# Kernel optimization log

Hardware: AMD Instinct MI355X
Metric: run time of the kernel (lower is better)

The kernel has to match this reference:

```python
import jax, jax.numpy as jnp
import numpy as np

WEIGHT = 1.0
SIM_THRESHOLD = 0.8


def setup_inputs() -> dict:
    key = jax.random.key(0)
    k1, k2, k3, k4 = jax.random.split(key, 4)
    B, E, H, C = 8192, 16, 1024, 128  # batch, num_experts, hidden, clusters
    routing_probs = jax.random.normal(k1, (B, E), dtype=jnp.float32)
    # Clustered embeddings so some pairs exceed the similarity threshold:
    # intra-cluster cosine sim ~ 1024/(1024 + 0.09*1024) ~ 0.92 > 0.8.
    centers = jax.random.normal(k2, (C, H), dtype=jnp.float32)
    assign = jax.random.randint(k3, (B,), 0, C)
    input_embeddings = centers[assign] + 0.3 * jax.random.normal(k4, (B, H), dtype=jnp.float32)
    return {"routing_probs": routing_probs, "input_embeddings": input_embeddings}


def reference(routing_probs, input_embeddings):
    B = routing_probs.shape[0]
    # L2-normalize embeddings and build pairwise cosine similarity [B, B]
    emb = input_embeddings / jnp.linalg.norm(input_embeddings, axis=-1, keepdims=True)
    sim = emb @ emb.T
    mask = (sim > SIM_THRESHOLD) & ~jnp.eye(B, dtype=bool)
    # Batch-wide softmax/log_softmax computed once (fuses the per-pair loop)
    L = jax.nn.log_softmax(routing_probs, axis=-1)  # [B, E]
    P = jnp.exp(L)                                   # [B, E]
    neg_entropy = jnp.sum(P * L, axis=-1)            # [B], sum_k p_j log p_j
    # kl[i, j] = KL(P_j || P_i) = sum_k P_j (log P_j - L_i)
    kl = neg_entropy[None, :] - L @ P.T              # [B, B]
    cnt = jnp.sum(mask)
    loss = jnp.where(
        cnt > 0,
        jnp.sum(jnp.where(mask, kl, 0.0)) / jnp.maximum(cnt, 1).astype(kl.dtype),
        jnp.array(0.0, dtype=kl.dtype),
    )
    return WEIGHT * loss
```

## Files before the change

kernel.cpp:

```cpp
#include <hip/hip_runtime.h>
#include <hip/hip_bf16.h>
#include <math.h>

#define B_SZ 8192
#define H_SZ 1024
#define E_SZ 16
#define SIM_THR 0.8f

typedef float floatx4 __attribute__((ext_vector_type(4)));
typedef long  longx2  __attribute__((ext_vector_type(2)));

#define OFF_NE   4096
#define OFF_L    65536
#define OFF_P    (65536 + 524288)
#define OFF_EMB  2097152


__device__ __forceinline__ void gload16(const void* g, void* l) {
    __builtin_amdgcn_global_load_lds(
        (const __attribute__((address_space(1))) void*)g,
        (__attribute__((address_space(3))) void*)l, 16, 0, 0);
}

__global__ void prep_kernel(const float* __restrict__ rp,
                            const float* __restrict__ emb,
                            unsigned char* __restrict__ out8,
                            float* __restrict__ L, float* __restrict__ P,
                            float* __restrict__ ne,
                            float* __restrict__ gsum, unsigned int* __restrict__ gcnt,
                            unsigned int* __restrict__ done) {
    const int b = blockIdx.x;
    if (b < 2048) {
        int r    = b * 4 + (threadIdx.x >> 6);
        int lane = threadIdx.x & 63;
        int kt = lane >> 2, q = lane & 3;
        const float4* row4 = (const float4*)(emb + (size_t)r * H_SZ);
        int f0 = (kt * 64 + q * 8) >> 2;
        float4 a0 = row4[f0],     a1 = row4[f0 + 1];
        float4 b0 = row4[f0 + 8], b1 = row4[f0 + 9];
        float ss = a0.x*a0.x + a0.y*a0.y + a0.z*a0.z + a0.w*a0.w
                 + a1.x*a1.x + a1.y*a1.y + a1.z*a1.z + a1.w*a1.w
                 + b0.x*b0.x + b0.y*b0.y + b0.z*b0.z + b0.w*b0.w
                 + b1.x*b1.x + b1.y*b1.y + b1.z*b1.z + b1.w*b1.w;
#pragma unroll
        for (int off = 32; off > 0; off >>= 1) ss += __shfl_down(ss, off, 64);
        ss = __shfl(ss, 0, 64);
        float inv = rsqrtf(ss);
        unsigned int w0, w1, w2, w3;
        w0 = (unsigned int)__builtin_amdgcn_cvt_pk_fp8_f32(a0.x * inv, a0.y * inv, 0, false);
        w0 = (unsigned int)__builtin_amdgcn_cvt_pk_fp8_f32(a0.z * inv, a0.w * inv, w0, true);
        w1 = (unsigned int)__builtin_amdgcn_cvt_pk_fp8_f32(a1.x * inv, a1.y * inv, 0, false);
        w1 = (unsigned int)__builtin_amdgcn_cvt_pk_fp8_f32(a1.z * inv, a1.w * inv, w1, true);
        w2 = (unsigned int)__builtin_amdgcn_cvt_pk_fp8_f32(b0.x * inv, b0.y * inv, 0, false);
        w2 = (unsigned int)__builtin_amdgcn_cvt_pk_fp8_f32(b0.z * inv, b0.w * inv, w2, true);
        w3 = (unsigned int)__builtin_amdgcn_cvt_pk_fp8_f32(b1.x * inv, b1.y * inv, 0, false);
        w3 = (unsigned int)__builtin_amdgcn_cvt_pk_fp8_f32(b1.z * inv, b1.w * inv, w3, true);
        size_t dst = (size_t)(r >> 4) * 16384 + (size_t)kt * 1024
                   + (size_t)q * 256 + (size_t)(r & 15) * 16;
        uint4 c = {w0, w1, w2, w3};
        *(uint4*)(out8 + dst) = c;
    } else {
        int i = (b - 2048) * 256 + threadIdx.x;
        if (i == 0) { *gsum = 0.f; *gcnt = 0u; *done = 0u; }
        if (i >= B_SZ) return;
        const float* x = rp + i * E_SZ;
        float v[E_SZ];
        float m = -INFINITY;
#pragma unroll
        for (int k = 0; k < E_SZ; k++) { v[k] = x[k]; m = fmaxf(m, v[k]); }
        float s = 0.f;
#pragma unroll
        for (int k = 0; k < E_SZ; k++) s += expf(v[k] - m);
        float lse = m + logf(s);
        float nent = 0.f;
#pragma unroll
        for (int k = 0; k < E_SZ; k++) {
            float l = v[k] - lse;
            float p = expf(l);
            L[i * E_SZ + k] = l;
            P[i * E_SZ + k] = p;
            nent += p * l;
        }
        ne[i] = nent;
    }
}

__device__ __forceinline__ int cnt_range(int lo, int hi, int r, int* first) {
    int lo2 = lo + ((r - lo) & 7);
    *first = lo2;
    return (lo2 > hi) ? 0 : ((hi - lo2) >> 3) + 1;
}

#define GRID_PER_XCD 164
__global__ __launch_bounds__(512, 4)
void sim_kl_kernel(const unsigned char* __restrict__ embL,
                   const float* __restrict__ Lm, const float* __restrict__ Pm,
                   const float* __restrict__ ne,
                   float* __restrict__ gsum, unsigned int* __restrict__ gcnt,
                   unsigned int* __restrict__ done, float* __restrict__ out) {
    __shared__ __align__(16) char As[2][16384];
    __shared__ __align__(16) char Bs[2][8192];
    __shared__ float redf[8];
    __shared__ unsigned int redc[8];

    const int x = blockIdx.x & 7;
    int s = blockIdx.x >> 3;
    int BI = 0, bj = 0;
    bool have = false;
    for (BI = 0; BI < 32; BI++) {
        int lo = 2 * BI, f1, f2;
        int n1 = (lo <= 31) ? cnt_range(lo, 31, x, &f1) : 0;
        int n2 = cnt_range(lo < 32 ? 32 : lo, 63, 7 - x, &f2);
        if (s < n1) { bj = f1 + 8 * s; have = true; break; }
        s -= n1;
        if (s < n2) { bj = f2 + 8 * s; have = true; break; }
        s -= n2;
    }

    const int tid  = threadIdx.x;
    const int lane = tid & 63;
    const int wave = tid >> 6;

    float fsum = 0.f;
    unsigned int lcnt = 0;

    if (have) {
        const int rowI = BI * 256, rowJ = bj * 128;
        const int wrg = (wave >> 1);
        const int wcg = (wave & 1);
        const int quad = lane >> 4;
        const int l16  = lane & 15;

        floatx4 acc[4][4];
#pragma unroll
        for (int mi = 0; mi < 4; mi++)
#pragma unroll
            for (int ni = 0; ni < 4; ni++) {
                floatx4 z = {0.f, 0.f, 0.f, 0.f};
                acc[mi][ni] = z;
            }

        const char* srcA = (const char*)embL + (size_t)(BI * 16 + 2 * wave) * 16384 + lane * 16;
        const char* srcB = (const char*)embL + (size_t)(bj * 8 + wave) * 16384 + lane * 16;
        const int aW = 2 * wave * 1024;
        const int bW = wave * 1024;

        {
            gload16(srcA,         As[0] + aW);
            gload16(srcA + 16384, As[0] + aW + 1024);
            gload16(srcB,         Bs[0] + bW);
        }

        const int aoff = wrg * 4096 + lane * 16;
        const int boff = wcg * 4096 + lane * 16;

        for (int kt = 0; kt < 16; kt++) {
            const int b = kt & 1;
            __syncthreads();
            if (kt + 1 < 16) {
                const int ko = (kt + 1) * 1024;
                gload16(srcA + ko,         As[b ^ 1] + aW);
                gload16(srcA + ko + 16384, As[b ^ 1] + aW + 1024);
                gload16(srcB + ko,         Bs[b ^ 1] + bW);
            }

            longx2 af[4], bfm[4];
#pragma unroll
            for (int mi = 0; mi < 4; mi++)
                af[mi] = *(const longx2*)(As[b] + aoff + mi * 1024);
#pragma unroll
            for (int ni = 0; ni < 4; ni++)
                bfm[ni] = *(const longx2*)(Bs[b] + boff + ni * 1024);
#pragma unroll
            for (int mi = 0; mi < 4; mi++)
#pragma unroll
                for (int ni = 0; ni < 4; ni++) {
                    acc[mi][ni] = __builtin_amdgcn_mfma_f32_16x16x32_fp8_fp8(
                        af[mi].x, bfm[ni].x, acc[mi][ni], 0, 0, 0);
                    acc[mi][ni] = __builtin_amdgcn_mfma_f32_16x16x32_fp8_fp8(
                        af[mi].y, bfm[ni].y, acc[mi][ni], 0, 0, 0);
                }
        }

        __syncthreads();
        unsigned short* wl = (unsigned short*)As + wave * 2048;
        int base = 0;
#pragma unroll
        for (int mi = 0; mi < 4; mi++) {
#pragma unroll
            for (int ni = 0; ni < 4; ni++) {
#pragma unroll
                for (int r = 0; r < 4; r++) {
                    int il = wrg * 64 + mi * 16 + quad * 4 + r;
                    int jl = wcg * 64 + ni * 16 + l16;
                    bool msk = (acc[mi][ni][r] > SIM_THR) && (rowJ + jl > rowI + il);
                    unsigned long long bal = __ballot(msk);
                    if (msk) {
                        int pos = base + __popcll(bal & ((1ull << lane) - 1ull));
                        if (pos < 2048) wl[pos] = (unsigned short)((il << 7) | jl);
                    }
                    base += __popcll(bal);
                }
            }
        }
        if (base > 2048) base = 2048;

        for (int t = lane; t < base; t += 64) {
            int e = wl[t];
            int i = rowI + (e >> 7), j = rowJ + (e & 127);
            const float4* Li4 = (const float4*)(Lm + i * E_SZ);
            const float4* Pj4 = (const float4*)(Pm + j * E_SZ);
            const float4* Lj4 = (const float4*)(Lm + j * E_SZ);
            const float4* Pi4 = (const float4*)(Pm + i * E_SZ);
            float d = 0.f, d2 = 0.f;
#pragma unroll
            for (int q = 0; q < 4; q++) {
                float4 a = Li4[q], bb = Pj4[q];
                d += a.x * bb.x + a.y * bb.y + a.z * bb.z + a.w * bb.w;
                float4 a2 = Lj4[q], b2 = Pi4[q];
                d2 += a2.x * b2.x + a2.y * b2.y + a2.z * b2.z + a2.w * b2.w;
            }
            fsum += (ne[j] - d) + (ne[i] - d2);
            lcnt += 2;
        }
    }

#pragma unroll
    for (int off = 32; off > 0; off >>= 1) {
        fsum += __shfl_down(fsum, off, 64);
        lcnt += __shfl_down(lcnt, off, 64);
    }
    if (lane == 0) { redf[wave] = fsum; redc[wave] = lcnt; }
    __syncthreads();
    if (tid == 0) {
        float sv = 0.f;
        unsigned int c = 0u;
#pragma unroll
        for (int w = 0; w < 8; w++) { sv += redf[w]; c += redc[w]; }
        if (c > 0u) {
            atomicAdd(gsum, sv);
            atomicAdd(gcnt, c);
        }
        __threadfence();
        unsigned int old = atomicAdd(done, 1u);
        if (old == gridDim.x - 1) {
            float S = atomicAdd(gsum, 0.0f);
            unsigned int C = atomicAdd(gcnt, 0u);
            out[0] = (C > 0u) ? (S / (float)C) : 0.f;
        }
    }
}

extern "C" void kernel_launch(void* const* d_in, const int* in_sizes, int n_in,
                              void* d_out, int out_size, void* d_ws, size_t ws_size,
                              hipStream_t stream) {
    const float* rp  = (const float*)d_in[0];
    const float* emb = (const float*)d_in[1];
    float* out = (float*)d_out;

    char* ws = (char*)d_ws;
    float*         gsum = (float*)(ws + 0);
    unsigned int*  gcnt = (unsigned int*)(ws + 4);
    unsigned int*  done = (unsigned int*)(ws + 8);
    float*         ne   = (float*)(ws + OFF_NE);
    float*         Lm   = (float*)(ws + OFF_L);
    float*         Pm   = (float*)(ws + OFF_P);
    unsigned char* embL = (unsigned char*)(ws + OFF_EMB);

    prep_kernel<<<2048 + 32, 256, 0, stream>>>(rp, emb, embL, Lm, Pm, ne, gsum, gcnt, done);
    sim_kl_kernel<<<8 * GRID_PER_XCD, 512, 0, stream>>>(embL, Lm, Pm, ne, gsum, gcnt, done, out);
}
```

Before: 174.2 us.

## Switch similarity GEMM from fp8 to int8 MFMA with LDS-staged prep

Embeddings are quantized to symmetric int8 (scaled by 127 after L2 normalization) instead of fp8. The similarity tiles are computed with the i32 16x16x64 int8 MFMA, and the threshold is compared as an integer (0.8*127^2). The prep kernel now handles 16 rows per block and stages them in LDS so the tiled layout is written with coalesced stores. Together this halves the MFMA instruction count per k-tile and makes prep writes cheaper, at the cost of int8 quantization error near the threshold.

```diff
diff --git a/kernel.cpp b/kernel.cpp
--- a/kernel.cpp
+++ b/kernel.cpp
@@ -5,10 +5,9 @@
 #define B_SZ 8192
 #define H_SZ 1024
 #define E_SZ 16
-#define SIM_THR 0.8f
-
+#define SIM_THR_I 12903
 typedef float floatx4 __attribute__((ext_vector_type(4)));
-typedef long  longx2  __attribute__((ext_vector_type(2)));
+typedef int   intx4   __attribute__((ext_vector_type(4)));
 
 #define OFF_NE   4096
 #define OFF_L    65536
@@ -22,45 +21,58 @@
         (__attribute__((address_space(3))) void*)l, 16, 0, 0);
 }
 
-__global__ void prep_kernel(const float* __restrict__ rp,
-                            const float* __restrict__ emb,
-                            unsigned char* __restrict__ out8,
-                            float* __restrict__ L, float* __restrict__ P,
-                            float* __restrict__ ne,
-                            float* __restrict__ gsum, unsigned int* __restrict__ gcnt,
-                            unsigned int* __restrict__ done) {
+__device__ __forceinline__ unsigned int pack4_i8(float4 v, float s) {
+    int a = (int)rintf(v.x * s), b = (int)rintf(v.y * s);
+    int c = (int)rintf(v.z * s), d = (int)rintf(v.w * s);
+    return (a & 255) | ((b & 255) << 8) | ((c & 255) << 16) | ((d & 255) << 24);
+}
+
+__global__ __launch_bounds__(256)
+void prep_kernel(const float* __restrict__ rp,
+                 const float* __restrict__ emb,
+                 unsigned char* __restrict__ out8,
+                 float* __restrict__ L, float* __restrict__ P,
+                 float* __restrict__ ne,
+                 float* __restrict__ gsum, unsigned int* __restrict__ gcnt,
+                 unsigned int* __restrict__ done) {
     const int b = blockIdx.x;
-    if (b < 2048) {
-        int r    = b * 4 + (threadIdx.x >> 6);
-        int lane = threadIdx.x & 63;
-        int kt = lane >> 2, q = lane & 3;
-        const float4* row4 = (const float4*)(emb + (size_t)r * H_SZ);
-        int f0 = (kt * 64 + q * 8) >> 2;
-        float4 a0 = row4[f0],     a1 = row4[f0 + 1];
-        float4 b0 = row4[f0 + 8], b1 = row4[f0 + 9];
-        float ss = a0.x*a0.x + a0.y*a0.y + a0.z*a0.z + a0.w*a0.w
-                 + a1.x*a1.x + a1.y*a1.y + a1.z*a1.z + a1.w*a1.w
-                 + b0.x*b0.x + b0.y*b0.y + b0.z*b0.z + b0.w*b0.w
-                 + b1.x*b1.x + b1.y*b1.y + b1.z*b1.z + b1.w*b1.w;
-#pragma unroll
-        for (int off = 32; off > 0; off >>= 1) ss += __shfl_down(ss, off, 64);
-        ss = __shfl(ss, 0, 64);
-        float inv = rsqrtf(ss);
-        unsigned int w0, w1, w2, w3;
-        w0 = (unsigned int)__builtin_amdgcn_cvt_pk_fp8_f32(a0.x * inv, a0.y * inv, 0, false);
-        w0 = (unsigned int)__builtin_amdgcn_cvt_pk_fp8_f32(a0.z * inv, a0.w * inv, w0, true);
-        w1 = (unsigned int)__builtin_amdgcn_cvt_pk_fp8_f32(a1.x * inv, a1.y * inv, 0, false);
-        w1 = (unsigned int)__builtin_amdgcn_cvt_pk_fp8_f32(a1.z * inv, a1.w * inv, w1, true);
-        w2 = (unsigned int)__builtin_amdgcn_cvt_pk_fp8_f32(b0.x * inv, b0.y * inv, 0, false);
-        w2 = (unsigned int)__builtin_amdgcn_cvt_pk_fp8_f32(b0.z * inv, b0.w * inv, w2, true);
-        w3 = (unsigned int)__builtin_amdgcn_cvt_pk_fp8_f32(b1.x * inv, b1.y * inv, 0, false);
-        w3 = (unsigned int)__builtin_amdgcn_cvt_pk_fp8_f32(b1.z * inv, b1.w * inv, w3, true);
-        size_t dst = (size_t)(r >> 4) * 16384 + (size_t)kt * 1024
-                   + (size_t)q * 256 + (size_t)(r & 15) * 16;
-        uint4 c = {w0, w1, w2, w3};
-        *(uint4*)(out8 + dst) = c;
+    const int tid = threadIdx.x;
+    if (b < 512) {
+        __shared__ __align__(16) unsigned char stage[16 * 1040];
+        const int wave = tid >> 6, lane = tid & 63;
+        const int g = b;
+#pragma unroll
+        for (int t = 0; t < 4; t++) {
+            int r = g * 16 + wave * 4 + t;
+            const float4* row4 = (const float4*)(emb + (size_t)r * H_SZ);
+            float4 v0 = row4[lane * 4 + 0], v1 = row4[lane * 4 + 1];
+            float4 v2 = row4[lane * 4 + 2], v3 = row4[lane * 4 + 3];
+            float ss = v0.x*v0.x + v0.y*v0.y + v0.z*v0.z + v0.w*v0.w
+                     + v1.x*v1.x + v1.y*v1.y + v1.z*v1.z + v1.w*v1.w
+                     + v2.x*v2.x + v2.y*v2.y + v2.z*v2.z + v2.w*v2.w
+                     + v3.x*v3.x + v3.y*v3.y + v3.z*v3.z + v3.w*v3.w;
+#pragma unroll
+            for (int off = 32; off > 0; off >>= 1) ss += __shfl_down(ss, off, 64);
+            ss = __shfl(ss, 0, 64);
+            float s = rsqrtf(ss) * 127.0f;
+            uint4 c;
+            c.x = pack4_i8(v0, s);
+            c.y = pack4_i8(v1, s);
+            c.z = pack4_i8(v2, s);
+            c.w = pack4_i8(v3, s);
+            *(uint4*)(stage + (r & 15) * 1040 + lane * 16) = c;
+        }
+        __syncthreads();
+#pragma unroll
+        for (int p = 0; p < 4; p++) {
+            int d = p * 256 + tid;
+            int m = d & 15;
+            int c = (d >> 6) * 4 + ((d >> 4) & 3);
+            uint4 v = *(const uint4*)(stage + m * 1040 + c * 16);
+            *(uint4*)(out8 + (size_t)g * 16384 + (size_t)d * 16) = v;
+        }
     } else {
-        int i = (b - 2048) * 256 + threadIdx.x;
+        int i = (b - 512) * 256 + tid;
         if (i == 0) { *gsum = 0.f; *gcnt = 0u; *done = 0u; }
         if (i >= B_SZ) return;
         const float* x = rp + i * E_SZ;
@@ -131,12 +143,12 @@
         const int quad = lane >> 4;
         const int l16  = lane & 15;
 
-        floatx4 acc[4][4];
+        intx4 acc[4][4];
 #pragma unroll
         for (int mi = 0; mi < 4; mi++)
 #pragma unroll
             for (int ni = 0; ni < 4; ni++) {
-                floatx4 z = {0.f, 0.f, 0.f, 0.f};
+                intx4 z = {0, 0, 0, 0};
                 acc[mi][ni] = z;
             }
 
@@ -164,22 +176,19 @@
                 gload16(srcB + ko,         Bs[b ^ 1] + bW);
             }
 
-            longx2 af[4], bfm[4];
+            intx4 af[4], bf[4];
 #pragma unroll
             for (int mi = 0; mi < 4; mi++)
-                af[mi] = *(const longx2*)(As[b] + aoff + mi * 1024);
+                af[mi] = *(const intx4*)(As[b] + aoff + mi * 1024);
 #pragma unroll
             for (int ni = 0; ni < 4; ni++)
-                bfm[ni] = *(const longx2*)(Bs[b] + boff + ni * 1024);
+                bf[ni] = *(const intx4*)(Bs[b] + boff + ni * 1024);
 #pragma unroll
             for (int mi = 0; mi < 4; mi++)
 #pragma unroll
-                for (int ni = 0; ni < 4; ni++) {
-                    acc[mi][ni] = __builtin_amdgcn_mfma_f32_16x16x32_fp8_fp8(
-                        af[mi].x, bfm[ni].x, acc[mi][ni], 0, 0, 0);
-                    acc[mi][ni] = __builtin_amdgcn_mfma_f32_16x16x32_fp8_fp8(
-                        af[mi].y, bfm[ni].y, acc[mi][ni], 0, 0, 0);
-                }
+                for (int ni = 0; ni < 4; ni++)
+                    acc[mi][ni] = __builtin_amdgcn_mfma_i32_16x16x64_i8(
+                        af[mi], bf[ni], acc[mi][ni], 0, 0, 0);
         }
 
         __syncthreads();
@@ -193,7 +202,7 @@
                 for (int r = 0; r < 4; r++) {
                     int il = wrg * 64 + mi * 16 + quad * 4 + r;
                     int jl = wcg * 64 + ni * 16 + l16;
-                    bool msk = (acc[mi][ni][r] > SIM_THR) && (rowJ + jl > rowI + il);
+                    bool msk = (acc[mi][ni][r] > SIM_THR_I) && (rowJ + jl > rowI + il);
                     unsigned long long bal = __ballot(msk);
                     if (msk) {
                         int pos = base + __popcll(bal & ((1ull << lane) - 1ull));
@@ -267,6 +276,6 @@
     float*         Pm   = (float*)(ws + OFF_P);
     unsigned char* embL = (unsigned char*)(ws + OFF_EMB);
 
-    prep_kernel<<<2048 + 32, 256, 0, stream>>>(rp, emb, embL, Lm, Pm, ne, gsum, gcnt, done);
+    prep_kernel<<<512 + 32, 256, 0, stream>>>(rp, emb, embL, Lm, Pm, ne, gsum, gcnt, done);
     sim_kl_kernel<<<8 * GRID_PER_XCD, 512, 0, stream>>>(embL, Lm, Pm, ne, gsum, gcnt, done, out);
 }
```

Result: faster. 165.6 us (-4.9%).
